# Kernel tuning notes

Measured on AMD Instinct MI355X. Metric: run time of the kernel, lower is better.

## Reference

```python
import jax, jax.numpy as jnp
import numpy as np

B, P, V, L = 256, 512, 8, 16
N = B * P            # 131072 nodes
C = V * L            # 128 in_channels (== out_channels, forced by the .view in forward)
H = 4                # heads
DOUT = 128           # out_channels per head
E = N * 5            # k=5 neighbors per node
NEG_SLOPE = 0.2


def setup_inputs() -> dict:
    key = jax.random.key(0)
    ks = jax.random.split(key, 8)
    patches = jax.random.normal(ks[0], (B, P, V, L), dtype=jnp.float32)
    edge_index = jax.random.randint(ks[1], (2, E), 0, N, dtype=jnp.int64)
    s = 1.0 / np.sqrt(C)
    W_gat = jax.random.uniform(ks[2], (C, H * DOUT), dtype=jnp.float32, minval=-s, maxval=s)
    att_src = jax.random.uniform(ks[3], (H, DOUT), dtype=jnp.float32, minval=-s, maxval=s)
    att_dst = jax.random.uniform(ks[4], (H, DOUT), dtype=jnp.float32, minval=-s, maxval=s)
    bias_gat = jnp.zeros((H * DOUT,), dtype=jnp.float32)
    s2 = 1.0 / np.sqrt(H * DOUT)
    W_lin = jax.random.uniform(ks[5], (H * DOUT, DOUT), dtype=jnp.float32, minval=-s2, maxval=s2)
    b_lin = jax.random.uniform(ks[6], (DOUT,), dtype=jnp.float32, minval=-s2, maxval=s2)
    return {"patches": patches, "edge_index": edge_index, "W_gat": W_gat,
            "att_src": att_src, "att_dst": att_dst, "bias_gat": bias_gat,
            "W_lin": W_lin, "b_lin": b_lin}


def reference(patches, edge_index, W_gat, att_src, att_dst, bias_gat, W_lin, b_lin):
    b, p, v, l = patches.shape
    n = b * p
    x = patches.reshape(n, v * l)                      # [N, C]
    xw = (x @ W_gat).reshape(n, H, DOUT)               # [N, H, D]
    # PyG GATConv default add_self_loops=True
    loops = jnp.arange(n, dtype=edge_index.dtype)
    src = jnp.concatenate([edge_index[0], loops])      # message source j
    dst = jnp.concatenate([edge_index[1], loops])      # message target i
    a_src = jnp.einsum('nhd,hd->nh', xw, att_src)      # [N, H]
    a_dst = jnp.einsum('nhd,hd->nh', xw, att_dst)
    e = jax.nn.leaky_relu(a_src[src] + a_dst[dst], NEG_SLOPE)   # [Etot, H]
    m = jax.ops.segment_max(e, dst, num_segments=n)
    ex = jnp.exp(e - m[dst])
    denom = jax.ops.segment_sum(ex, dst, num_segments=n)
    alpha = ex / (denom[dst] + 1e-16)                  # segment softmax over in-edges
    out = jax.ops.segment_sum(alpha[:, :, None] * xw[src], dst, num_segments=n)  # [N, H, D]
    out = out.reshape(n, H * DOUT) + bias_gat
    out = jax.nn.elu(out)
    out = out @ W_lin + b_lin                          # [N, DOUT]
    return out.reshape(b, p, v, l)
```

## Files before the change

kernel.cpp:

```cpp
#include <hip/hip_runtime.h>
#include <hip/hip_bf16.h>
#include <stdint.h>

#define N_NODES 131072
#define C_IN    128
#define HEADS   4
#define DHEAD   128
#define HD      512
#define E_EDGES 655360
#define NEG_SLOPE 0.2f
#define SCAN_B  (N_NODES / 256)
#define MT      32

typedef short bf16x8 __attribute__((ext_vector_type(8)));
typedef float f32x4  __attribute__((ext_vector_type(4)));

__device__ __forceinline__ float bf2f(unsigned short u) {
    unsigned int x = ((unsigned int)u) << 16;
    return __builtin_bit_cast(float, x);
}
__device__ __forceinline__ unsigned short f2bf(float f) {
    unsigned int u = __builtin_bit_cast(unsigned int, f);
    unsigned int r = u + 0x7FFFu + ((u >> 16) & 1u);
    return (unsigned short)(r >> 16);
}
__device__ __forceinline__ float lrelu(float v) {
    return v > 0.0f ? v : NEG_SLOPE * v;
}

__device__ __forceinline__ int perm512(int s) {
    int w = s >> 7, r = s & 127;
    int P = r >> 5, half = (r >> 3) & 3, b = (r >> 2) & 1, e = r & 3;
    return w * 128 + (2 * P + b) * 16 + half * 4 + e;
}

__global__ void detect_kernel(const unsigned int* p_f, const unsigned int* p_i, int* flags) {
    int lane = threadIdx.x;
    int cnt = 0;
#pragma unroll
    for (int r = 0; r < 4; r++) {
        unsigned int e = (p_f[lane + 64 * r] >> 7) & 0xFFu;
        cnt += (e >= 110u && e <= 137u) ? 1 : 0;
    }
    int z = 0;
#pragma unroll
    for (int r = 0; r < 2; r++) {
        z += (p_i[2 * (lane + 64 * r) + 1] == 0u) ? 1 : 0;
    }
#pragma unroll
    for (int o = 1; o < 64; o <<= 1) {
        cnt += __shfl_xor(cnt, o, 64);
        z   += __shfl_xor(z, o, 64);
    }
    if (lane == 0) {
        flags[0] = (cnt >= 128) ? 1 : 0;
        flags[1] = (z == 128) ? 1 : 0;
    }
}

__global__ void conv_w1(const void* in, unsigned short* out, const int* flags) {
    int idx = blockIdx.x * blockDim.x + threadIdx.x;
    int e = idx & 7;
    int l = (idx >> 3) & 63;
    int t = idx >> 9;
    int kk = t & 3, g = t >> 2;
    int col = g * 16 + (l & 15);
    int k = kk * 32 + (l >> 4) * 8 + e;
    float v = flags[0] ? bf2f(((const unsigned short*)in)[k * HD + col])
                       : ((const float*)in)[k * HD + col];
    out[idx] = f2bf(v);
}

__global__ void conv_w2(const void* in, unsigned short* out, const int* flags) {
    int idx = blockIdx.x * blockDim.x + threadIdx.x;
    int e = idx & 7;
    int l = (idx >> 3) & 63;
    int f = idx >> 9;
    int kk = f & 15, jg = f >> 4;
    int col = jg * 16 + (l & 15);
    int sk = kk * 32 + (l >> 4) * 8 + e;
    int k = perm512(sk);
    float v = flags[0] ? bf2f(((const unsigned short*)in)[k * DHEAD + col])
                       : ((const float*)in)[k * DHEAD + col];
    out[idx] = f2bf(v);
}

__global__ void conv_small(const void* as, const void* ad, const void* bg, const void* bl,
                           float* att_s, float* att_d, float* bias_g, float* b_lin,
                           const int* flags) {
    int i = blockIdx.x * blockDim.x + threadIdx.x;
    bool bf = flags[0] != 0;
    if (i < 512) {
        att_s[i] = bf ? bf2f(((const unsigned short*)as)[i]) : ((const float*)as)[i];
    } else if (i < 1024) {
        int j = i - 512;
        att_d[j] = bf ? bf2f(((const unsigned short*)ad)[j]) : ((const float*)ad)[j];
    } else if (i < 1536) {
        int j = perm512(i - 1024);
        bias_g[i - 1024] = bf ? bf2f(((const unsigned short*)bg)[j]) : ((const float*)bg)[j];
    } else if (i < 1664) {
        int j = i - 1536;
        b_lin[j] = bf ? bf2f(((const unsigned short*)bl)[j]) : ((const float*)bl)[j];
    }
}

__global__ void conv_edges_hist(const void* in, int* src32, int* dst32, int* deg,
                                const int* flags) {
    int i = blockIdx.x * blockDim.x + threadIdx.x;
    if (i >= 2 * E_EDGES) return;
    int v = flags[1] ? (int)((const long long*)in)[i] : ((const int*)in)[i];
    if (i < E_EDGES) {
        src32[i] = v;
    } else {
        dst32[i - E_EDGES] = v;
        atomicAdd(&deg[v], 1);
    }
}

__global__ void zero_deg(int* deg) {
    int i = blockIdx.x * blockDim.x + threadIdx.x;
    deg[i] = 0;
}

__global__ void scan_local(const int* __restrict__ deg, int* __restrict__ offv,
                           int* __restrict__ bsums) {
    __shared__ int tmp[256];
    int t = threadIdx.x;
    int g = blockIdx.x * 256 + t;
    int v = deg[g];
    tmp[t] = v;
    __syncthreads();
#pragma unroll
    for (int d = 1; d < 256; d <<= 1) {
        int x = (t >= d) ? tmp[t - d] : 0;
        __syncthreads();
        tmp[t] += x;
        __syncthreads();
    }
    offv[g] = tmp[t] - v;
    if (t == 255) bsums[blockIdx.x] = tmp[t];
}

__global__ void scan_bsums(int* bsums) {
    __shared__ int tmp[SCAN_B];
    int t = threadIdx.x;
    int v = bsums[t];
    tmp[t] = v;
    __syncthreads();
#pragma unroll
    for (int d = 1; d < SCAN_B; d <<= 1) {
        int x = (t >= d) ? tmp[t - d] : 0;
        __syncthreads();
        tmp[t] += x;
        __syncthreads();
    }
    bsums[t] = tmp[t] - v;
}

__global__ void scan_apply(int* __restrict__ offv, const int* __restrict__ bsums,
                           int* __restrict__ cursor) {
    int g = blockIdx.x * 256 + threadIdx.x;
    int v = offv[g] + bsums[blockIdx.x];
    offv[g] = v;
    cursor[g] = v;
}

__global__ void scatter_kernel(const int* src32, const int* dst32, int* cursor, int* csr) {
    int i = blockIdx.x * blockDim.x + threadIdx.x;
    int d = dst32[i];
    int pos = atomicAdd(&cursor[d], 1);
    csr[pos] = src32[i];
}

__launch_bounds__(256)
__global__ void gemm1_fused(const void* __restrict__ Ain,
                            const unsigned short* __restrict__ BT2,
                            const float* __restrict__ attS, const float* __restrict__ attD,
                            unsigned short* __restrict__ xw,
                            float* __restrict__ aSrc, float* __restrict__ aDst,
                            const int* __restrict__ flags) {
    __shared__ unsigned short lA[64 * 136];
    int tid = threadIdx.x;
    int m0 = blockIdx.x * 64;

    if (flags[0] == 0) {
        const float* Af = (const float*)Ain;
#pragma unroll
        for (int p = 0; p < 8; p++) {
            int l = p * 256 + tid;
            int r = l >> 5, c = (l & 31) * 4;
            float4 f = *(const float4*)&Af[(size_t)(m0 + r) * C_IN + c];
            unsigned short t4[4] = {f2bf(f.x), f2bf(f.y), f2bf(f.z), f2bf(f.w)};
            *(uint2*)&lA[r * 136 + c] = *(const uint2*)t4;
        }
    } else {
        const unsigned short* Ab = (const unsigned short*)Ain;
#pragma unroll
        for (int p = 0; p < 4; p++) {
            int l = p * 256 + tid;
            int r = l >> 4, c = (l & 15) * 8;
            *(uint4*)&lA[r * 136 + c] = *(const uint4*)&Ab[(size_t)(m0 + r) * C_IN + c];
        }
    }
    __syncthreads();

    int w = tid >> 6, lane = tid & 63;
    int lr = lane & 15, half = lane >> 4;

    bf16x8 afr[4][4];
#pragma unroll
    for (int i = 0; i < 4; i++)
#pragma unroll
        for (int kk = 0; kk < 4; kk++)
            afr[i][kk] = *(const bf16x8*)&lA[(i * 16 + lr) * 136 + kk * 32 + half * 8];

    const float4* attS4 = (const float4*)attS;
    const float4* attD4 = (const float4*)attD;

    float dS[4], dD[4];
#pragma unroll
    for (int i = 0; i < 4; i++) { dS[i] = 0.f; dD[i] = 0.f; }

    bf16x8 bbuf[2][4];
#pragma unroll
    for (int kk = 0; kk < 4; kk++)
        bbuf[0][kk] = *(const bf16x8*)&BT2[(((w * 8 + 0) * 4 + kk) << 9) + (lane << 3)];

    uint2 pk_lo[4];

#pragma unroll
    for (int p = 0; p < 8; p++) {
        int cur = p & 1;
        if (p < 7) {
#pragma unroll
            for (int kk = 0; kk < 4; kk++)
                bbuf[cur ^ 1][kk] =
                    *(const bf16x8*)&BT2[(((w * 8 + p + 1) * 4 + kk) << 9) + (lane << 3)];
        }

        f32x4 acc[4];
#pragma unroll
        for (int i = 0; i < 4; i++) acc[i] = (f32x4){0.f, 0.f, 0.f, 0.f};

#pragma unroll
        for (int kk = 0; kk < 4; kk++)
#pragma unroll
            for (int i = 0; i < 4; i++)
                acc[i] = __builtin_amdgcn_mfma_f32_16x16x32_bf16(bbuf[cur][kk], afr[i][kk], acc[i], 0, 0, 0);

        float4 s4 = attS4[w * 32 + p * 4 + half];
        float4 d4 = attD4[w * 32 + p * 4 + half];
#pragma unroll
        for (int i = 0; i < 4; i++) {
            dS[i] += acc[i][0] * s4.x + acc[i][1] * s4.y + acc[i][2] * s4.z + acc[i][3] * s4.w;
            dD[i] += acc[i][0] * d4.x + acc[i][1] * d4.y + acc[i][2] * d4.z + acc[i][3] * d4.w;
        }

        if ((p & 1) == 0) {
#pragma unroll
            for (int i = 0; i < 4; i++) {
                pk_lo[i].x = (unsigned int)f2bf(acc[i][0]) | ((unsigned int)f2bf(acc[i][1]) << 16);
                pk_lo[i].y = (unsigned int)f2bf(acc[i][2]) | ((unsigned int)f2bf(acc[i][3]) << 16);
            }
        } else {
            int P = p >> 1;
#pragma unroll
            for (int i = 0; i < 4; i++) {
                uint4 q;
                q.x = pk_lo[i].x;
                q.y = pk_lo[i].y;
                q.z = (unsigned int)f2bf(acc[i][0]) | ((unsigned int)f2bf(acc[i][1]) << 16);
                q.w = (unsigned int)f2bf(acc[i][2]) | ((unsigned int)f2bf(acc[i][3]) << 16);
                *(uint4*)&xw[(size_t)(m0 + i * 16 + lr) * HD + w * 128 + P * 32 + half * 8] = q;
            }
        }
    }

#pragma unroll
    for (int i = 0; i < 4; i++) {
        float ps = dS[i], pd = dD[i];
        ps += __shfl_xor(ps, 16, 64);
        ps += __shfl_xor(ps, 32, 64);
        pd += __shfl_xor(pd, 16, 64);
        pd += __shfl_xor(pd, 32, 64);
        if (half == 0) {
            aSrc[(size_t)(m0 + i * 16 + lr) * HEADS + w] = ps;
            aDst[(size_t)(m0 + i * 16 + lr) * HEADS + w] = pd;
        }
    }
}

__launch_bounds__(256)
__global__ void agg_gemm2(const unsigned short* __restrict__ xw,
                          const float* __restrict__ a_src, const float* __restrict__ a_dst,
                          const int* __restrict__ off, const int* __restrict__ deg,
                          const int* __restrict__ csr, const float* __restrict__ bias_g,
                          const unsigned short* __restrict__ BT2f,
                          const float* __restrict__ b_lin,
                          unsigned short* __restrict__ Cbf, float* __restrict__ Cf,
                          const int* __restrict__ flags) {
    __shared__ unsigned short yt[MT * 520];
    int tid = threadIdx.x;
    int m0 = blockIdx.x * MT;
    int w = tid >> 6, l = tid & 63;
    int h = l >> 4;
    int ebase = l * 8;

    for (int g = 0; g < MT / 4; g++) {
        int row = w * (MT / 4) + g;
        int node = m0 + row;
        int o = off[node], dn = deg[node];
        float ad = a_dst[node * HEADS + h];

        float acc[8];
        float denom;
        {
            float wgt = __expf(lrelu(a_src[node * HEADS + h] + ad));
            uint4 q = *(const uint4*)&xw[(size_t)node * HD + ebase];
            const unsigned short* u = (const unsigned short*)&q;
            denom = wgt;
#pragma unroll
            for (int k = 0; k < 8; k++) acc[k] = wgt * bf2f(u[k]);
        }

        for (int e0 = 0; e0 < dn; e0 += 8) {
            int   idx[8];
            float as[8];
            uint4 px[8];
#pragma unroll
            for (int b = 0; b < 8; b++)
                idx[b] = (e0 + b < dn) ? csr[o + e0 + b] : node;
#pragma unroll
            for (int b = 0; b < 8; b++)
                as[b] = a_src[idx[b] * HEADS + h];
#pragma unroll
            for (int b = 0; b < 8; b++)
                px[b] = *(const uint4*)&xw[(size_t)idx[b] * HD + ebase];
#pragma unroll
            for (int b = 0; b < 8; b++) {
                float wgt = (e0 + b < dn) ? __expf(lrelu(as[b] + ad)) : 0.0f;
                denom += wgt;
                const unsigned short* u = (const unsigned short*)&px[b];
#pragma unroll
                for (int k = 0; k < 8; k++) acc[k] += wgt * bf2f(u[k]);
            }
        }

        float inv = 1.0f / (denom + 1e-16f);
        unsigned short outp[8];
#pragma unroll
        for (int k = 0; k < 8; k++) {
            float v = acc[k] * inv + bias_g[ebase + k];
            v = v > 0.f ? v : (__expf(v) - 1.0f);
            outp[k] = f2bf(v);
        }
        *(uint4*)&yt[row * 520 + ebase] = *(const uint4*)outp;
    }
    __syncthreads();

    int lr = l & 15, half = l >> 4;
    f32x4 acc2[2][2];
#pragma unroll
    for (int i = 0; i < 2; i++)
#pragma unroll
        for (int j = 0; j < 2; j++) acc2[i][j] = (f32x4){0.f, 0.f, 0.f, 0.f};

    bf16x8 bb[2][2];
#pragma unroll
    for (int j = 0; j < 2; j++)
        bb[0][j] = *(const bf16x8*)&BT2f[((((w * 2 + j) * 16 + 0) * 64 + l) << 3)];

    for (int kk = 0; kk < 16; kk++) {
        int cur = kk & 1;
        if (kk < 15) {
#pragma unroll
            for (int j = 0; j < 2; j++)
                bb[cur ^ 1][j] = *(const bf16x8*)&BT2f[((((w * 2 + j) * 16 + kk + 1) * 64 + l) << 3)];
        }
        bf16x8 af0 = *(const bf16x8*)&yt[(lr) * 520 + kk * 32 + half * 8];
        bf16x8 af1 = *(const bf16x8*)&yt[(16 + lr) * 520 + kk * 32 + half * 8];
        acc2[0][0] = __builtin_amdgcn_mfma_f32_16x16x32_bf16(af0, bb[cur][0], acc2[0][0], 0, 0, 0);
        acc2[0][1] = __builtin_amdgcn_mfma_f32_16x16x32_bf16(af0, bb[cur][1], acc2[0][1], 0, 0, 0);
        acc2[1][0] = __builtin_amdgcn_mfma_f32_16x16x32_bf16(af1, bb[cur][0], acc2[1][0], 0, 0, 0);
        acc2[1][1] = __builtin_amdgcn_mfma_f32_16x16x32_bf16(af1, bb[cur][1], acc2[1][1], 0, 0, 0);
    }

    if (flags[0] != 0) {
        __syncthreads();
#pragma unroll
        for (int i = 0; i < 2; i++)
#pragma unroll
            for (int j = 0; j < 2; j++) {
                int gcol = (w * 2 + j) * 16 + lr;
                float b = b_lin[gcol];
#pragma unroll
                for (int r = 0; r < 4; r++)
                    yt[(i * 16 + half * 4 + r) * 136 + gcol] = f2bf(acc2[i][j][r] + b);
            }
        __syncthreads();
#pragma unroll
        for (int p = 0; p < 2; p++) {
            int ln = p * 256 + tid;
            int r = ln >> 4, c = (ln & 15) * 8;
            *(uint4*)&Cbf[(size_t)(m0 + r) * DHEAD + c] = *(const uint4*)&yt[r * 136 + c];
        }
    } else {
#pragma unroll
        for (int i = 0; i < 2; i++)
#pragma unroll
            for (int j = 0; j < 2; j++) {
                int gcol = (w * 2 + j) * 16 + lr;
                float b = b_lin[gcol];
#pragma unroll
                for (int r = 0; r < 4; r++) {
                    int grow = m0 + i * 16 + half * 4 + r;
                    Cf[(size_t)grow * DHEAD + gcol] = acc2[i][j][r] + b;
                }
            }
    }
}

extern "C" void kernel_launch(void* const* d_in, const int* in_sizes, int n_in,
                              void* d_out, int out_size, void* d_ws, size_t ws_size,
                              hipStream_t stream) {
    char* ws = (char*)d_ws;
    size_t wsoff = 0;
    auto alloc = [&](size_t bytes) -> char* {
        char* p = ws + wsoff;
        wsoff += (bytes + 255) & ~(size_t)255;
        return p;
    };

    int*            flags  = (int*)           alloc(256);
    unsigned short* WT1    = (unsigned short*)alloc((size_t)HD * C_IN * 2);
    unsigned short* WT2    = (unsigned short*)alloc((size_t)DHEAD * HD * 2);
    float*          attS   = (float*)         alloc(HD * 4);
    float*          attD   = (float*)         alloc(HD * 4);
    float*          biasG  = (float*)         alloc(HD * 4);
    float*          bLin   = (float*)         alloc(DHEAD * 4);
    int*            src32  = (int*)           alloc((size_t)E_EDGES * 4);
    int*            dst32  = (int*)           alloc((size_t)E_EDGES * 4);
    int*            deg    = (int*)           alloc((size_t)N_NODES * 4);
    int*            offv   = (int*)           alloc((size_t)(N_NODES + 1) * 4);
    int*            cursor = (int*)           alloc((size_t)N_NODES * 4);
    int*            csr    = (int*)           alloc((size_t)E_EDGES * 4);
    int*            bsums  = (int*)           alloc((size_t)SCAN_B * 4);
    float*          aSrc   = (float*)         alloc((size_t)N_NODES * HEADS * 4);
    float*          aDst   = (float*)         alloc((size_t)N_NODES * HEADS * 4);
    unsigned short* xw     = (unsigned short*)alloc((size_t)N_NODES * HD * 2);

    const void* patches = d_in[0];
    const void* edges   = d_in[1];
    const void* Wgat    = d_in[2];
    const void* attSrcI = d_in[3];
    const void* attDstI = d_in[4];
    const void* biasGI  = d_in[5];
    const void* WlinI   = d_in[6];
    const void* bLinI   = d_in[7];

    detect_kernel<<<1, 64, 0, stream>>>((const unsigned int*)patches,
                                        (const unsigned int*)edges, flags);

    conv_w1<<<(HD * C_IN) / 256, 256, 0, stream>>>(Wgat, WT1, flags);
    conv_w2<<<(DHEAD * HD) / 256, 256, 0, stream>>>(WlinI, WT2, flags);
    conv_small<<<7, 256, 0, stream>>>(attSrcI, attDstI, biasGI, bLinI,
                                      attS, attD, biasG, bLin, flags);

    zero_deg<<<N_NODES / 256, 256, 0, stream>>>(deg);
    conv_edges_hist<<<(2 * E_EDGES) / 256, 256, 0, stream>>>(edges, src32, dst32, deg, flags);
    scan_local<<<SCAN_B, 256, 0, stream>>>(deg, offv, bsums);
    scan_bsums<<<1, SCAN_B, 0, stream>>>(bsums);
    scan_apply<<<SCAN_B, 256, 0, stream>>>(offv, bsums, cursor);
    scatter_kernel<<<E_EDGES / 256, 256, 0, stream>>>(src32, dst32, cursor, csr);

    gemm1_fused<<<N_NODES / 64, 256, 0, stream>>>(
        patches, WT1, attS, attD, xw, aSrc, aDst, flags);

    agg_gemm2<<<N_NODES / MT, 256, 0, stream>>>(
        xw, aSrc, aDst, offv, deg, csr, biasG, WT2, bLin,
        (unsigned short*)d_out, (float*)d_out, flags);
}
```

Measured before the change: 387.4 us.

## Use 512-thread blocks in agg_gemm2 and skip padded neighbor loads

The fused aggregation/GEMM2 kernel now runs with 8 waves per block instead of 4. Each wave aggregates 4 rows instead of 8, and in the MFMA stage each wave computes one 16-column tile instead of two. Padded neighbor slots no longer load the node's own features redundantly; the loads are predicated off and replaced with zeros. The aim is more latency hiding for the gather-bound aggregation, at the cost of halving per-wave MFMA work and possibly raising register pressure under the new launch bounds.

```diff
diff --git a/kernel.cpp b/kernel.cpp
--- a/kernel.cpp
+++ b/kernel.cpp
@@ -290,7 +290,7 @@
     }
 }
 
-__launch_bounds__(256)
+__launch_bounds__(512)
 __global__ void agg_gemm2(const unsigned short* __restrict__ xw,
                           const float* __restrict__ a_src, const float* __restrict__ a_dst,
                           const int* __restrict__ off, const int* __restrict__ deg,
@@ -306,8 +306,8 @@
     int h = l >> 4;
     int ebase = l * 8;
 
-    for (int g = 0; g < MT / 4; g++) {
-        int row = w * (MT / 4) + g;
+    for (int g = 0; g < MT / 8; g++) {
+        int row = w * (MT / 8) + g;
         int node = m0 + row;
         int o = off[node], dn = deg[node];
         float ad = a_dst[node * HEADS + h];
@@ -329,13 +329,17 @@
             uint4 px[8];
 #pragma unroll
             for (int b = 0; b < 8; b++)
-                idx[b] = (e0 + b < dn) ? csr[o + e0 + b] : node;
+                idx[b] = (e0 + b < dn) ? csr[o + e0 + b] : 0;
 #pragma unroll
             for (int b = 0; b < 8; b++)
-                as[b] = a_src[idx[b] * HEADS + h];
-#pragma unroll
-            for (int b = 0; b < 8; b++)
-                px[b] = *(const uint4*)&xw[(size_t)idx[b] * HD + ebase];
+                as[b] = (e0 + b < dn) ? a_src[idx[b] * HEADS + h] : 0.0f;
+#pragma unroll
+            for (int b = 0; b < 8; b++) {
+                if (e0 + b < dn)
+                    px[b] = *(const uint4*)&xw[(size_t)idx[b] * HD + ebase];
+                else
+                    px[b] = (uint4){0u, 0u, 0u, 0u};
+            }
 #pragma unroll
             for (int b = 0; b < 8; b++) {
                 float wgt = (e0 + b < dn) ? __expf(lrelu(as[b] + ad)) : 0.0f;
@@ -359,64 +363,49 @@
     __syncthreads();
 
     int lr = l & 15, half = l >> 4;
-    f32x4 acc2[2][2];
-#pragma unroll
-    for (int i = 0; i < 2; i++)
-#pragma unroll
-        for (int j = 0; j < 2; j++) acc2[i][j] = (f32x4){0.f, 0.f, 0.f, 0.f};
-
-    bf16x8 bb[2][2];
-#pragma unroll
-    for (int j = 0; j < 2; j++)
-        bb[0][j] = *(const bf16x8*)&BT2f[((((w * 2 + j) * 16 + 0) * 64 + l) << 3)];
+    f32x4 acc2[2];
+    acc2[0] = (f32x4){0.f, 0.f, 0.f, 0.f};
+    acc2[1] = (f32x4){0.f, 0.f, 0.f, 0.f};
+
+    bf16x8 bcur = *(const bf16x8*)&BT2f[(((w * 16 + 0) * 64 + l) << 3)];
 
     for (int kk = 0; kk < 16; kk++) {
-        int cur = kk & 1;
-        if (kk < 15) {
-#pragma unroll
-            for (int j = 0; j < 2; j++)
-                bb[cur ^ 1][j] = *(const bf16x8*)&BT2f[((((w * 2 + j) * 16 + kk + 1) * 64 + l) << 3)];
-        }
+        bf16x8 bnext;
+        if (kk < 15)
+            bnext = *(const bf16x8*)&BT2f[(((w * 16 + kk + 1) * 64 + l) << 3)];
         bf16x8 af0 = *(const bf16x8*)&yt[(lr) * 520 + kk * 32 + half * 8];
         bf16x8 af1 = *(const bf16x8*)&yt[(16 + lr) * 520 + kk * 32 + half * 8];
-        acc2[0][0] = __builtin_amdgcn_mfma_f32_16x16x32_bf16(af0, bb[cur][0], acc2[0][0], 0, 0, 0);
-        acc2[0][1] = __builtin_amdgcn_mfma_f32_16x16x32_bf16(af0, bb[cur][1], acc2[0][1], 0, 0, 0);
-        acc2[1][0] = __builtin_amdgcn_mfma_f32_16x16x32_bf16(af1, bb[cur][0], acc2[1][0], 0, 0, 0);
-        acc2[1][1] = __builtin_amdgcn_mfma_f32_16x16x32_bf16(af1, bb[cur][1], acc2[1][1], 0, 0, 0);
+        acc2[0] = __builtin_amdgcn_mfma_f32_16x16x32_bf16(af0, bcur, acc2[0], 0, 0, 0);
+        acc2[1] = __builtin_amdgcn_mfma_f32_16x16x32_bf16(af1, bcur, acc2[1], 0, 0, 0);
+        bcur = bnext;
     }
 
     if (flags[0] != 0) {
         __syncthreads();
 #pragma unroll
-        for (int i = 0; i < 2; i++)
-#pragma unroll
-            for (int j = 0; j < 2; j++) {
-                int gcol = (w * 2 + j) * 16 + lr;
-                float b = b_lin[gcol];
-#pragma unroll
-                for (int r = 0; r < 4; r++)
-                    yt[(i * 16 + half * 4 + r) * 136 + gcol] = f2bf(acc2[i][j][r] + b);
+        for (int i = 0; i < 2; i++) {
+            int gcol = w * 16 + lr;
+            float b = b_lin[gcol];
+#pragma unroll
+            for (int r = 0; r < 4; r++)
+                yt[(i * 16 + half * 4 + r) * 136 + gcol] = f2bf(acc2[i][r] + b);
+        }
+        __syncthreads();
+        {
+            int r = tid >> 4, c = (tid & 15) * 8;
+            *(uint4*)&Cbf[(size_t)(m0 + r) * DHEAD + c] = *(const uint4*)&yt[r * 136 + c];
+        }
+    } else {
+#pragma unroll
+        for (int i = 0; i < 2; i++) {
+            int gcol = w * 16 + lr;
+            float b = b_lin[gcol];
+#pragma unroll
+            for (int r = 0; r < 4; r++) {
+                int grow = m0 + i * 16 + half * 4 + r;
+                Cf[(size_t)grow * DHEAD + gcol] = acc2[i][r] + b;
             }
-        __syncthreads();
-#pragma unroll
-        for (int p = 0; p < 2; p++) {
-            int ln = p * 256 + tid;
-            int r = ln >> 4, c = (ln & 15) * 8;
-            *(uint4*)&Cbf[(size_t)(m0 + r) * DHEAD + c] = *(const uint4*)&yt[r * 136 + c];
-        }
-    } else {
-#pragma unroll
-        for (int i = 0; i < 2; i++)
-#pragma unroll
-            for (int j = 0; j < 2; j++) {
-                int gcol = (w * 2 + j) * 16 + lr;
-                float b = b_lin[gcol];
-#pragma unroll
-                for (int r = 0; r < 4; r++) {
-                    int grow = m0 + i * 16 + half * 4 + r;
-                    Cf[(size_t)grow * DHEAD + gcol] = acc2[i][j][r] + b;
-                }
-            }
+        }
     }
 }
 
@@ -476,7 +465,7 @@
     gemm1_fused<<<N_NODES / 64, 256, 0, stream>>>(
         patches, WT1, attS, attD, xw, aSrc, aDst, flags);
 
-    agg_gemm2<<<N_NODES / MT, 256, 0, stream>>>(
+    agg_gemm2<<<N_NODES / MT, 512, 0, stream>>>(
         xw, aSrc, aDst, offv, deg, csr, biasG, WT2, bLin,
         (unsigned short*)d_out, (float*)d_out, flags);
 }
```

After: 418.3 us. +8.0%, slower.
